# Kernel optimization log

Hardware: AMD Instinct MI355X
Metric: run time of the kernel (lower is better)

The kernel has to match this reference:

```python
import jax, jax.numpy as jnp
import numpy as np

N = 62      # EEG channels / graph nodes
F = 5       # features per node (frequency bands)
H = 64      # num_hiddens
C = 3       # num_classes
K = 2       # SGC propagation steps
B = 32768   # batch size
BN_EPS = 1e-5
NORM_EPS = 1e-10


def setup_inputs() -> dict:
    key = jax.random.key(0)
    ks = jax.random.split(key, 8)
    n_tril = N * (N + 1) // 2  # 1953 lower-tri (incl diag) learnable edge weights
    return {
        "X": jax.random.normal(ks[0], (B, N, F), dtype=jnp.float32),
        "edge_w_tril": jax.random.normal(ks[1], (n_tril,), dtype=jnp.float32),
        "bn_gamma": jnp.ones((F,), dtype=jnp.float32),
        "bn_beta": jnp.zeros((F,), dtype=jnp.float32),
        "lin_W": jax.random.normal(ks[2], (F, H), dtype=jnp.float32) * 0.1,
        "lin_b": jax.random.normal(ks[3], (H,), dtype=jnp.float32) * 0.1,
        "fc1_W": jax.random.normal(ks[4], (N * H, 64), dtype=jnp.float32) * 0.02,
        "fc1_b": jax.random.normal(ks[5], (64,), dtype=jnp.float32) * 0.02,
        "fc2_W": jax.random.normal(ks[6], (64, C), dtype=jnp.float32) * 0.1,
        "fc2_b": jax.random.normal(ks[7], (C,), dtype=jnp.float32) * 0.1,
    }


def _propagation_matrix(edge_w_tril):
    # Rebuild symmetric learnable adjacency from lower-tri params
    xs, ys = jnp.tril_indices(N)
    W = jnp.zeros((N, N), dtype=edge_w_tril.dtype).at[xs, ys].set(edge_w_tril)
    W = W + W.T - jnp.diag(jnp.diag(W))
    # normalize_A: relu + D^{-1/2} A D^{-1/2}
    A = jax.nn.relu(W)
    d = jnp.sum(A, axis=1)
    dinv = 1.0 / jnp.sqrt(d + NORM_EPS)
    L = dinv[:, None] * A * dinv[None, :]
    # NewSGConv.norm: add self-loops (weight 1), deg = row-sum of |w|,
    # norm_ij = deg_i^{-1/2} w_ij deg_j^{-1/2}. Dense form since edge list is all-pairs.
    deg = jnp.sum(jnp.abs(L), axis=1) + 1.0  # +1 from self-loop
    dis = 1.0 / jnp.sqrt(deg)                 # deg >= 1, no inf
    S = dis[:, None] * (L + jnp.eye(N, dtype=L.dtype)) * dis[None, :]
    return S


def _forward(X, edge_w_tril, bn_gamma, bn_beta, lin_W, lin_b, fc1_W, fc1_b, fc2_W, fc2_b):
    # BatchNorm1d over feature dim (training mode: batch stats over (B, N)), biased var
    mean = jnp.mean(X, axis=(0, 1))
    var = jnp.mean(jnp.square(X - mean), axis=(0, 1))
    x = (X - mean) / jnp.sqrt(var + BN_EPS) * bn_gamma + bn_beta  # (B, N, F)

    S = _propagation_matrix(edge_w_tril)  # (N, N)
    # K steps of SGC propagation: x <- S x (gather-scale-scatter == dense matmul here)
    for _ in range(K):
        x = jnp.einsum('ij,bjf->bif', S, x)
    x = jnp.einsum('bnf,fh->bnh', x, lin_W) + lin_b  # SGConv linear, (B, N, H)

    x = x.reshape(x.shape[0], -1)                    # (B, N*H)
    x = jax.nn.relu(x @ fc1_W + fc1_b)
    return x @ fc2_W + fc2_b                         # (B, C) logits


def reference(X, edge_w_tril, bn_gamma, bn_beta, lin_W, lin_b, fc1_W, fc1_b, fc2_W, fc2_b):
    return _forward(X, edge_w_tril, bn_gamma, bn_beta, lin_W, lin_b,
                    fc1_W, fc1_b, fc2_W, fc2_b)
```

## Files before the change

### kernel.cpp

```cpp
#include <hip/hip_runtime.h>
#include <math.h>


typedef __bf16 bf16_t;
typedef __attribute__((ext_vector_type(8))) __bf16 bf16x8;
typedef __attribute__((ext_vector_type(4))) float f32x4;

#define BN_COUNT 2031616.0f

__global__ __launch_bounds__(256) void k_conv(const float* __restrict__ X,
                                              const float* __restrict__ edge,
                                              float* __restrict__ part,
                                              bf16x8* __restrict__ Ahi,
                                              bf16x8* __restrict__ Alo,
                                              float* __restrict__ S2g)
{
    __shared__ float lds[32 * 312];
    const int t = threadIdx.x;
    if (blockIdx.x < 1024) {
        const float* Xb = X + (size_t)blockIdx.x * 32 * 310;
        float s0=0,s1=0,s2=0,s3=0,s4=0,q0=0,q1=0,q2=0,q3=0,q4=0;
        for (int i = t; i < 4960; i += 256) {
            int row = i / 155;
            int cc  = i - row * 155;
            float2 v = *reinterpret_cast<const float2*>(Xb + (size_t)row*310 + 2*cc);
            lds[row*312 + 2*cc]     = v.x;
            lds[row*312 + 2*cc + 1] = v.y;
            int f0 = (2*cc) % 5;
            int f1 = (f0 == 4) ? 0 : f0 + 1;
            float xx = v.x*v.x, yy = v.y*v.y;
            s0 += (f0==0)?v.x:0.f; s1 += (f0==1)?v.x:0.f; s2 += (f0==2)?v.x:0.f;
            s3 += (f0==3)?v.x:0.f; s4 += (f0==4)?v.x:0.f;
            q0 += (f0==0)?xx:0.f;  q1 += (f0==1)?xx:0.f;  q2 += (f0==2)?xx:0.f;
            q3 += (f0==3)?xx:0.f;  q4 += (f0==4)?xx:0.f;
            s0 += (f1==0)?v.y:0.f; s1 += (f1==1)?v.y:0.f; s2 += (f1==2)?v.y:0.f;
            s3 += (f1==3)?v.y:0.f; s4 += (f1==4)?v.y:0.f;
            q0 += (f1==0)?yy:0.f;  q1 += (f1==1)?yy:0.f;  q2 += (f1==2)?yy:0.f;
            q3 += (f1==3)?yy:0.f;  q4 += (f1==4)?yy:0.f;
        }
        float st[10] = {s0,s1,s2,s3,s4,q0,q1,q2,q3,q4};
#pragma unroll
        for (int k = 0; k < 10; ++k)
#pragma unroll
            for (int m = 32; m >= 1; m >>= 1) st[k] += __shfl_xor(st[k], m);
        __shared__ float red[4][10];
        int lane = t & 63, w = t >> 6;
        if (lane == 0)
#pragma unroll
            for (int k = 0; k < 10; ++k) red[w][k] = st[k];
        __syncthreads();
        if (t < 10)
            part[blockIdx.x*10 + t] = red[0][t] + red[1][t] + red[2][t] + red[3][t];
        const int mt0 = blockIdx.x * 2;
        for (int i = t; i < 1280; i += 256) {
            int mt   = i / 640;
            int rem  = i - mt * 640;
            int ks   = rem >> 6;
            int lane2 = rem & 63;
            int row  = (mt << 4) + (lane2 & 15);
            int k0   = ks * 32 + ((lane2 >> 4) << 3);
            bf16x8 h8, l8;
#pragma unroll
            for (int j = 0; j < 8; ++j) {
                int k = k0 + j;
                float val = (k < 310) ? lds[row*312 + k] : 0.f;
                __bf16 h = (__bf16)val;
                h8[j] = h;
                l8[j] = (__bf16)(val - (float)h);
            }
            size_t idx = (size_t)(mt0 + mt) * 640 + ks * 64 + lane2;
            Ahi[idx] = h8;
            Alo[idx] = l8;
        }
    } else {
        float* Sm  = lds;
        float* dv  = lds + 3968;
        float* dis = lds + 4032;
        for (int e = t; e < 3968; e += 256) {
            int i = e >> 6, j = e & 63;
            float v = 0.f;
            if (j < 62) {
                int idx = (i >= j) ? (i*(i+1)/2 + j) : (j*(j+1)/2 + i);
                v = fmaxf(edge[idx], 0.f);
            }
            Sm[e] = v;
        }
        __syncthreads();
        if (t < 62) {
            float s = 0.f;
            for (int j = 0; j < 64; ++j) s += Sm[t*64 + j];
            dv[t] = 1.0f / sqrtf(s + 1e-10f);
        }
        __syncthreads();
        for (int e = t; e < 3968; e += 256) {
            int i = e >> 6, j = e & 63;
            if (j < 62) Sm[e] *= dv[i] * dv[j];
        }
        __syncthreads();
        if (t < 62) {
            float dg = 1.0f;
            for (int j = 0; j < 64; ++j) dg += fabsf(Sm[t*64 + j]);
            dis[t] = 1.0f / sqrtf(dg);
        }
        __syncthreads();
        for (int e = t; e < 3968; e += 256) {
            int i = e >> 6, j = e & 63;
            if (j < 62) {
                float v = Sm[e] + ((i == j) ? 1.0f : 0.0f);
                Sm[e] = dis[i] * v * dis[j];
            }
        }
        __syncthreads();
        for (int g = t; g < 992; g += 256) {
            int i = g >> 4, j0 = (g & 15) << 2;
            float4 acc = {0.f, 0.f, 0.f, 0.f};
            for (int k = 0; k < 62; ++k) {
                float s = Sm[i*64 + k];
                float4 b = *reinterpret_cast<const float4*>(&Sm[k*64 + j0]);
                acc.x += s*b.x; acc.y += s*b.y; acc.z += s*b.z; acc.w += s*b.w;
            }
            *reinterpret_cast<float4*>(&S2g[i*64 + j0]) = acc;
        }
    }
}

__global__ __launch_bounds__(256) void k_setup(
    const float* __restrict__ part, const float* __restrict__ S2g,
    const float* __restrict__ gamma, const float* __restrict__ beta,
    const float* __restrict__ linW, const float* __restrict__ linb,
    const float* __restrict__ fc1W, const float* __restrict__ fc1b,
    float* __restrict__ MeffT, float* __restrict__ constv)
{
    const int o = blockIdx.x;
    const int t = threadIdx.x;
    __shared__ float S2m[3968];
    __shared__ float colo[3968];
    __shared__ float Tm[310];
    __shared__ float lw[320];
    __shared__ float scale[5], shift[5];
    __shared__ float redbuf[256];

    {
        float st[10];
#pragma unroll
        for (int k = 0; k < 10; ++k) st[k] = 0.f;
        for (int b = t; b < 1024; b += 256)
#pragma unroll
            for (int k = 0; k < 10; ++k) st[k] += part[b*10 + k];
#pragma unroll
        for (int k = 0; k < 10; ++k)
#pragma unroll
            for (int m = 32; m >= 1; m >>= 1) st[k] += __shfl_xor(st[k], m);
        int lane = t & 63, w = t >> 6;
        if (lane == 0)
            for (int k = 0; k < 10; ++k) redbuf[w*10 + k] = st[k];
    }
    for (int i = t; i < 3968; i += 256) {
        S2m[i]  = S2g[i];
        colo[i] = fc1W[(size_t)i*64 + o];
    }
    for (int i = t; i < 320; i += 256) lw[i] = linW[i];
    __syncthreads();

    if (t < 10)
        redbuf[64 + t] = redbuf[t] + redbuf[10+t] + redbuf[20+t] + redbuf[30+t];
    __syncthreads();
    if (t < 5) {
        float mean = redbuf[64 + t] * (1.0f / BN_COUNT);
        float var  = redbuf[69 + t] * (1.0f / BN_COUNT) - mean*mean;
        float inv  = 1.0f / sqrtf(var + 1e-5f);
        scale[t] = gamma[t] * inv;
        shift[t] = beta[t] - mean * gamma[t] * inv;
    }
    for (int p = t; p < 310; p += 256) {
        int n = p / 5, f = p - n*5;
        float sum = 0.f;
        for (int h = 0; h < 64; ++h) sum += lw[f*64 + h] * colo[n*64 + h];
        Tm[p] = sum;
    }
    __syncthreads();
    float cpart = 0.f;
    for (int p = t; p < 310; p += 256) {
        int j = p / 5, f = p - j*5;
        float m = 0.f;
        for (int n = 0; n < 62; ++n) m += S2m[n*64 + j] * Tm[n*5 + f];
        MeffT[o*320 + p] = scale[f] * m;
        cpart += shift[f] * m;
    }
    if (t < 10) MeffT[o*320 + 310 + t] = 0.f;
    for (int nh = t; nh < 3968; nh += 256)
        cpart += linb[nh & 63] * colo[nh];
    __syncthreads();
    redbuf[t] = cpart;
    __syncthreads();
    for (int sft = 128; sft > 0; sft >>= 1) {
        if (t < sft) redbuf[t] += redbuf[t + sft];
        __syncthreads();
    }
    if (t == 0) constv[o] = redbuf[0] + fc1b[o];
}

__global__ __launch_bounds__(64) void k_pack(const float* __restrict__ MeffT,
                                             bf16x8* __restrict__ Bhi,
                                             bf16x8* __restrict__ Blo)
{
    const int b  = blockIdx.x;
    const int nt = b / 10;
    const int ks = b - nt * 10;
    const int lane = threadIdx.x;
    const int col = nt*16 + (lane & 15);
    const int k0  = ks*32 + ((lane >> 4) << 3);
    bf16x8 h8, l8;
#pragma unroll
    for (int j = 0; j < 8; ++j) {
        float val = MeffT[col*320 + k0 + j];
        __bf16 h = (__bf16)val;
        h8[j] = h;
        l8[j] = (__bf16)(val - (float)h);
    }
    Bhi[(nt*10 + ks)*64 + lane] = h8;
    Blo[(nt*10 + ks)*64 + lane] = l8;
}

__global__ __launch_bounds__(256) void k_gemm(
    const bf16x8* __restrict__ Ahi, const bf16x8* __restrict__ Alo,
    const bf16x8* __restrict__ Bhi, const bf16x8* __restrict__ Blo,
    const float* __restrict__ constv, const float* __restrict__ fc2W,
    const float* __restrict__ fc2b, float* __restrict__ out)
{
    const int t = threadIdx.x;
    const int lane = t & 63;
    const int waveId = blockIdx.x * 4 + (t >> 6);
    const bf16x8* pAh = Ahi + (size_t)waveId * 1280 + lane;
    const bf16x8* pAl = Alo + (size_t)waveId * 1280 + lane;
    const bf16x8* pBh = Bhi + lane;
    const bf16x8* pBl = Blo + lane;

    f32x4 acc[2][4];
#pragma unroll
    for (int m = 0; m < 2; ++m)
#pragma unroll
        for (int n = 0; n < 4; ++n) acc[m][n] = (f32x4){0.f,0.f,0.f,0.f};

    bf16x8 ah[2][2], al[2][2], bh[2][4], bl[2][4];
#define LOAD_KS(B_, KS_) do {                                            \
        ah[B_][0] = pAh[(KS_)*64];        ah[B_][1] = pAh[640 + (KS_)*64]; \
        al[B_][0] = pAl[(KS_)*64];        al[B_][1] = pAl[640 + (KS_)*64]; \
        bh[B_][0] = pBh[(KS_)*64];        bh[B_][1] = pBh[(10+(KS_))*64];  \
        bh[B_][2] = pBh[(20+(KS_))*64];   bh[B_][3] = pBh[(30+(KS_))*64];  \
        bl[B_][0] = pBl[(KS_)*64];        bl[B_][1] = pBl[(10+(KS_))*64];  \
        bl[B_][2] = pBl[(20+(KS_))*64];   bl[B_][3] = pBl[(30+(KS_))*64];  \
    } while (0)

    LOAD_KS(0, 0);
#pragma unroll
    for (int ks = 0; ks < 10; ++ks) {
        if (ks < 9) {
            if ((ks & 1) == 0) LOAD_KS(1, ks + 1);
            else               LOAD_KS(0, ks + 1);
        }
        const int bb = ks & 1;
#pragma unroll
        for (int m = 0; m < 2; ++m)
#pragma unroll
            for (int n = 0; n < 4; ++n) {
                acc[m][n] = __builtin_amdgcn_mfma_f32_16x16x32_bf16(ah[bb][m], bh[bb][n], acc[m][n], 0, 0, 0);
                acc[m][n] = __builtin_amdgcn_mfma_f32_16x16x32_bf16(ah[bb][m], bl[bb][n], acc[m][n], 0, 0, 0);
                acc[m][n] = __builtin_amdgcn_mfma_f32_16x16x32_bf16(al[bb][m], bh[bb][n], acc[m][n], 0, 0, 0);
            }
    }
#undef LOAD_KS

    const int cl = lane & 15;
    float cst[4], f2r[4][3];
#pragma unroll
    for (int n = 0; n < 4; ++n) {
        int col = n*16 + cl;
        cst[n]    = constv[col];
        f2r[n][0] = fc2W[col*3 + 0];
        f2r[n][1] = fc2W[col*3 + 1];
        f2r[n][2] = fc2W[col*3 + 2];
    }
    float b0 = fc2b[0], b1 = fc2b[1], b2 = fc2b[2];
#pragma unroll
    for (int m = 0; m < 2; ++m) {
#pragma unroll
        for (int r = 0; r < 4; ++r) {
            float p0 = 0.f, p1 = 0.f, p2 = 0.f;
#pragma unroll
            for (int n = 0; n < 4; ++n) {
                float z = fmaxf(acc[m][n][r] + cst[n], 0.f);
                p0 += z * f2r[n][0];
                p1 += z * f2r[n][1];
                p2 += z * f2r[n][2];
            }
#pragma unroll
            for (int msk = 1; msk < 16; msk <<= 1) {
                p0 += __shfl_xor(p0, msk);
                p1 += __shfl_xor(p1, msk);
                p2 += __shfl_xor(p2, msk);
            }
            if (cl == 0) {
                int row = waveId*32 + m*16 + (lane >> 4)*4 + r;
                size_t rw = (size_t)row * 3;
                out[rw + 0] = p0 + b0;
                out[rw + 1] = p1 + b1;
                out[rw + 2] = p2 + b2;
            }
        }
    }
}

extern "C" void kernel_launch(void* const* d_in, const int* in_sizes, int n_in,
                              void* d_out, int out_size, void* d_ws, size_t ws_size,
                              hipStream_t stream)
{
    const float* X     = (const float*)d_in[0];
    const float* edge  = (const float*)d_in[1];
    const float* gamma = (const float*)d_in[2];
    const float* beta  = (const float*)d_in[3];
    const float* linW  = (const float*)d_in[4];
    const float* linb  = (const float*)d_in[5];
    const float* fc1W  = (const float*)d_in[6];
    const float* fc1b  = (const float*)d_in[7];
    const float* fc2W  = (const float*)d_in[8];
    const float* fc2b  = (const float*)d_in[9];
    float* out = (float*)d_out;
    float* ws  = (float*)d_ws;

    float*  part   = ws;
    float*  S2g    = ws + 10240;
    float*  MeffT  = ws + 14208;
    float*  constv = ws + 34688;
    bf16x8* Bhi    = (bf16x8*)(ws + 34816);
    bf16x8* Blo    = (bf16x8*)(ws + 45056);
    bf16x8* Ahi    = (bf16x8*)(ws + 65536);
    bf16x8* Alo    = (bf16x8*)(ws + 5308416);

    hipLaunchKernelGGL(k_conv,  dim3(1025), dim3(256), 0, stream,
                       X, edge, part, Ahi, Alo, S2g);
    hipLaunchKernelGGL(k_setup, dim3(64),   dim3(256), 0, stream,
                       part, S2g, gamma, beta, linW, linb, fc1W, fc1b, MeffT, constv);
    hipLaunchKernelGGL(k_pack,  dim3(40),   dim3(64),  0, stream, MeffT, Bhi, Blo);
    hipLaunchKernelGGL(k_gemm,  dim3(256),  dim3(256), 0, stream,
                       Ahi, Alo, Bhi, Blo, constv, fc2W, fc2b, out);
}
```

Measured before the change: 143.1 us.

## Read X directly in GEMM, drop A-staging buffers and fuse B packing into setup

The stats kernel now only computes BatchNorm partial sums with vectorized float4 loads, and no longer writes bf16 hi/lo copies of X to the workspace. The GEMM kernel loads X rows straight from global memory and splits them into hi/lo bf16 in registers. The separate pack kernel is gone because setup now writes the MFMA-layout B fragments directly. This removes a large intermediate write and reread plus one launch. In exchange X is read twice, the GEMM loads are uncoalesced float2 accesses with a 310-float row stride, and each wave now covers 16 rows instead of 32.

After: 129.2 us. 1.11x faster.

```diff
diff --git a/kernel.cpp b/kernel.cpp
--- a/kernel.cpp
+++ b/kernel.cpp
@@ -2,76 +2,46 @@
 #include <math.h>
 
 
-typedef __bf16 bf16_t;
 typedef __attribute__((ext_vector_type(8))) __bf16 bf16x8;
 typedef __attribute__((ext_vector_type(4))) float f32x4;
 
 #define BN_COUNT 2031616.0f
 
-__global__ __launch_bounds__(256) void k_conv(const float* __restrict__ X,
-                                              const float* __restrict__ edge,
-                                              float* __restrict__ part,
-                                              bf16x8* __restrict__ Ahi,
-                                              bf16x8* __restrict__ Alo,
-                                              float* __restrict__ S2g)
-{
-    __shared__ float lds[32 * 312];
+__global__ __launch_bounds__(256) void k_stats(const float* __restrict__ X,
+                                               const float* __restrict__ edge,
+                                               float* __restrict__ part,
+                                               float* __restrict__ S2g)
+{
+    __shared__ __align__(16) float lds[4160];
     const int t = threadIdx.x;
-    if (blockIdx.x < 1024) {
-        const float* Xb = X + (size_t)blockIdx.x * 32 * 310;
-        float s0=0,s1=0,s2=0,s3=0,s4=0,q0=0,q1=0,q2=0,q3=0,q4=0;
-        for (int i = t; i < 4960; i += 256) {
-            int row = i / 155;
-            int cc  = i - row * 155;
-            float2 v = *reinterpret_cast<const float2*>(Xb + (size_t)row*310 + 2*cc);
-            lds[row*312 + 2*cc]     = v.x;
-            lds[row*312 + 2*cc + 1] = v.y;
-            int f0 = (2*cc) % 5;
-            int f1 = (f0 == 4) ? 0 : f0 + 1;
-            float xx = v.x*v.x, yy = v.y*v.y;
-            s0 += (f0==0)?v.x:0.f; s1 += (f0==1)?v.x:0.f; s2 += (f0==2)?v.x:0.f;
-            s3 += (f0==3)?v.x:0.f; s4 += (f0==4)?v.x:0.f;
-            q0 += (f0==0)?xx:0.f;  q1 += (f0==1)?xx:0.f;  q2 += (f0==2)?xx:0.f;
-            q3 += (f0==3)?xx:0.f;  q4 += (f0==4)?xx:0.f;
-            s0 += (f1==0)?v.y:0.f; s1 += (f1==1)?v.y:0.f; s2 += (f1==2)?v.y:0.f;
-            s3 += (f1==3)?v.y:0.f; s4 += (f1==4)?v.y:0.f;
-            q0 += (f1==0)?yy:0.f;  q1 += (f1==1)?yy:0.f;  q2 += (f1==2)?yy:0.f;
-            q3 += (f1==3)?yy:0.f;  q4 += (f1==4)?yy:0.f;
-        }
-        float st[10] = {s0,s1,s2,s3,s4,q0,q1,q2,q3,q4};
-#pragma unroll
-        for (int k = 0; k < 10; ++k)
-#pragma unroll
-            for (int m = 32; m >= 1; m >>= 1) st[k] += __shfl_xor(st[k], m);
-        __shared__ float red[4][10];
+    if (blockIdx.x < 496) {
+        int tid = blockIdx.x * 256 + t;
+        const float4* Xv = reinterpret_cast<const float4*>(X) + (size_t)tid * 20;
+        float s[5] = {0.f,0.f,0.f,0.f,0.f};
+        float q[5] = {0.f,0.f,0.f,0.f,0.f};
+#pragma unroll
+        for (int v = 0; v < 20; ++v) {
+            float4 x = Xv[v];
+            s[(4*v+0)%5] += x.x; q[(4*v+0)%5] += x.x*x.x;
+            s[(4*v+1)%5] += x.y; q[(4*v+1)%5] += x.y*x.y;
+            s[(4*v+2)%5] += x.z; q[(4*v+2)%5] += x.z*x.z;
+            s[(4*v+3)%5] += x.w; q[(4*v+3)%5] += x.w*x.w;
+        }
+#pragma unroll
+        for (int k = 0; k < 5; ++k)
+#pragma unroll
+            for (int m = 32; m >= 1; m >>= 1) {
+                s[k] += __shfl_xor(s[k], m);
+                q[k] += __shfl_xor(q[k], m);
+            }
         int lane = t & 63, w = t >> 6;
-        if (lane == 0)
-#pragma unroll
-            for (int k = 0; k < 10; ++k) red[w][k] = st[k];
+        if (lane == 0) {
+#pragma unroll
+            for (int k = 0; k < 5; ++k) { lds[w*10+k] = s[k]; lds[w*10+5+k] = q[k]; }
+        }
         __syncthreads();
         if (t < 10)
-            part[blockIdx.x*10 + t] = red[0][t] + red[1][t] + red[2][t] + red[3][t];
-        const int mt0 = blockIdx.x * 2;
-        for (int i = t; i < 1280; i += 256) {
-            int mt   = i / 640;
-            int rem  = i - mt * 640;
-            int ks   = rem >> 6;
-            int lane2 = rem & 63;
-            int row  = (mt << 4) + (lane2 & 15);
-            int k0   = ks * 32 + ((lane2 >> 4) << 3);
-            bf16x8 h8, l8;
-#pragma unroll
-            for (int j = 0; j < 8; ++j) {
-                int k = k0 + j;
-                float val = (k < 310) ? lds[row*312 + k] : 0.f;
-                __bf16 h = (__bf16)val;
-                h8[j] = h;
-                l8[j] = (__bf16)(val - (float)h);
-            }
-            size_t idx = (size_t)(mt0 + mt) * 640 + ks * 64 + lane2;
-            Ahi[idx] = h8;
-            Alo[idx] = l8;
-        }
+            part[blockIdx.x*10 + t] = lds[t] + lds[10+t] + lds[20+t] + lds[30+t];
     } else {
         float* Sm  = lds;
         float* dv  = lds + 3968;
@@ -129,7 +99,8 @@
     const float* __restrict__ gamma, const float* __restrict__ beta,
     const float* __restrict__ linW, const float* __restrict__ linb,
     const float* __restrict__ fc1W, const float* __restrict__ fc1b,
-    float* __restrict__ MeffT, float* __restrict__ constv)
+    __bf16* __restrict__ Bhi, __bf16* __restrict__ Blo,
+    float* __restrict__ constv)
 {
     const int o = blockIdx.x;
     const int t = threadIdx.x;
@@ -144,7 +115,7 @@
         float st[10];
 #pragma unroll
         for (int k = 0; k < 10; ++k) st[k] = 0.f;
-        for (int b = t; b < 1024; b += 256)
+        for (int b = t; b < 496; b += 256)
 #pragma unroll
             for (int k = 0; k < 10; ++k) st[k] += part[b*10 + k];
 #pragma unroll
@@ -179,15 +150,30 @@
         Tm[p] = sum;
     }
     __syncthreads();
+    const int nt = o >> 4;
+    const int cl = o & 15;
     float cpart = 0.f;
     for (int p = t; p < 310; p += 256) {
-        int j = p / 5, f = p - j*5;
+        int nd = p / 5, f = p - nd*5;
         float m = 0.f;
-        for (int n = 0; n < 62; ++n) m += S2m[n*64 + j] * Tm[n*5 + f];
-        MeffT[o*320 + p] = scale[f] * m;
+        for (int n = 0; n < 62; ++n) m += S2m[n*64 + nd] * Tm[n*5 + f];
+        float val = scale[f] * m;
         cpart += shift[f] * m;
-    }
-    if (t < 10) MeffT[o*320 + 310 + t] = 0.f;
+        int ks = p >> 5, qq = (p >> 3) & 3, jj = p & 7;
+        int ln = (qq << 4) | cl;
+        size_t fo = ((size_t)(nt*10 + ks)*64 + ln)*8 + jj;
+        __bf16 h = (__bf16)val;
+        Bhi[fo] = h;
+        Blo[fo] = (__bf16)(val - (float)h);
+    }
+    if (t < 10) {
+        int p = 310 + t;
+        int ks = p >> 5, qq = (p >> 3) & 3, jj = p & 7;
+        int ln = (qq << 4) | cl;
+        size_t fo = ((size_t)(nt*10 + ks)*64 + ln)*8 + jj;
+        Bhi[fo] = (__bf16)0.f;
+        Blo[fo] = (__bf16)0.f;
+    }
     for (int nh = t; nh < 3968; nh += 256)
         cpart += linb[nh & 63] * colo[nh];
     __syncthreads();
@@ -200,30 +186,37 @@
     if (t == 0) constv[o] = redbuf[0] + fc1b[o];
 }
 
-__global__ __launch_bounds__(64) void k_pack(const float* __restrict__ MeffT,
-                                             bf16x8* __restrict__ Bhi,
-                                             bf16x8* __restrict__ Blo)
-{
-    const int b  = blockIdx.x;
-    const int nt = b / 10;
-    const int ks = b - nt * 10;
-    const int lane = threadIdx.x;
-    const int col = nt*16 + (lane & 15);
-    const int k0  = ks*32 + ((lane >> 4) << 3);
-    bf16x8 h8, l8;
+__device__ __forceinline__ void loadA(const float* __restrict__ xrow, int q,
+                                      int ks, bf16x8& ah, bf16x8& al)
+{
+    float v[8];
+    if (ks < 9 || q < 2) {
+        float2 a = *reinterpret_cast<const float2*>(xrow + ks*32);
+        float2 b = *reinterpret_cast<const float2*>(xrow + ks*32 + 2);
+        float2 c = *reinterpret_cast<const float2*>(xrow + ks*32 + 4);
+        float2 d = *reinterpret_cast<const float2*>(xrow + ks*32 + 6);
+        v[0]=a.x; v[1]=a.y; v[2]=b.x; v[3]=b.y;
+        v[4]=c.x; v[5]=c.y; v[6]=d.x; v[7]=d.y;
+    } else if (q == 2) {
+        float2 a = *reinterpret_cast<const float2*>(xrow + ks*32);
+        float2 b = *reinterpret_cast<const float2*>(xrow + ks*32 + 2);
+        float2 c = *reinterpret_cast<const float2*>(xrow + ks*32 + 4);
+        v[0]=a.x; v[1]=a.y; v[2]=b.x; v[3]=b.y;
+        v[4]=c.x; v[5]=c.y; v[6]=0.f; v[7]=0.f;
+    } else {
+#pragma unroll
+        for (int j = 0; j < 8; ++j) v[j] = 0.f;
+    }
 #pragma unroll
     for (int j = 0; j < 8; ++j) {
-        float val = MeffT[col*320 + k0 + j];
-        __bf16 h = (__bf16)val;
-        h8[j] = h;
-        l8[j] = (__bf16)(val - (float)h);
-    }
-    Bhi[(nt*10 + ks)*64 + lane] = h8;
-    Blo[(nt*10 + ks)*64 + lane] = l8;
+        __bf16 h = (__bf16)v[j];
+        ah[j] = h;
+        al[j] = (__bf16)(v[j] - (float)h);
+    }
 }
 
 __global__ __launch_bounds__(256) void k_gemm(
-    const bf16x8* __restrict__ Ahi, const bf16x8* __restrict__ Alo,
+    const float* __restrict__ X,
     const bf16x8* __restrict__ Bhi, const bf16x8* __restrict__ Blo,
     const float* __restrict__ constv, const float* __restrict__ fc2W,
     const float* __restrict__ fc2b, float* __restrict__ out)
@@ -231,51 +224,46 @@
     const int t = threadIdx.x;
     const int lane = t & 63;
     const int waveId = blockIdx.x * 4 + (t >> 6);
-    const bf16x8* pAh = Ahi + (size_t)waveId * 1280 + lane;
-    const bf16x8* pAl = Alo + (size_t)waveId * 1280 + lane;
+    const int rl = lane & 15;
+    const int q  = lane >> 4;
+    const float* xrow = X + (size_t)(waveId*16 + rl)*310 + q*8;
     const bf16x8* pBh = Bhi + lane;
     const bf16x8* pBl = Blo + lane;
 
-    f32x4 acc[2][4];
-#pragma unroll
-    for (int m = 0; m < 2; ++m)
-#pragma unroll
-        for (int n = 0; n < 4; ++n) acc[m][n] = (f32x4){0.f,0.f,0.f,0.f};
-
-    bf16x8 ah[2][2], al[2][2], bh[2][4], bl[2][4];
-#define LOAD_KS(B_, KS_) do {                                            \
-        ah[B_][0] = pAh[(KS_)*64];        ah[B_][1] = pAh[640 + (KS_)*64]; \
-        al[B_][0] = pAl[(KS_)*64];        al[B_][1] = pAl[640 + (KS_)*64]; \
-        bh[B_][0] = pBh[(KS_)*64];        bh[B_][1] = pBh[(10+(KS_))*64];  \
-        bh[B_][2] = pBh[(20+(KS_))*64];   bh[B_][3] = pBh[(30+(KS_))*64];  \
-        bl[B_][0] = pBl[(KS_)*64];        bl[B_][1] = pBl[(10+(KS_))*64];  \
-        bl[B_][2] = pBl[(20+(KS_))*64];   bl[B_][3] = pBl[(30+(KS_))*64];  \
+    f32x4 acc[4];
+#pragma unroll
+    for (int n = 0; n < 4; ++n) acc[n] = (f32x4){0.f,0.f,0.f,0.f};
+
+    bf16x8 ah[2], al[2], bh[2][4], bl[2][4];
+#define LOAD_B(B_, KS_) do {                                              \
+        bh[B_][0] = pBh[(KS_)*64];        bh[B_][1] = pBh[(10+(KS_))*64]; \
+        bh[B_][2] = pBh[(20+(KS_))*64];   bh[B_][3] = pBh[(30+(KS_))*64]; \
+        bl[B_][0] = pBl[(KS_)*64];        bl[B_][1] = pBl[(10+(KS_))*64]; \
+        bl[B_][2] = pBl[(20+(KS_))*64];   bl[B_][3] = pBl[(30+(KS_))*64]; \
     } while (0)
 
-    LOAD_KS(0, 0);
+    loadA(xrow, q, 0, ah[0], al[0]);
+    LOAD_B(0, 0);
 #pragma unroll
     for (int ks = 0; ks < 10; ++ks) {
+        const int cur = ks & 1, nxt = cur ^ 1;
         if (ks < 9) {
-            if ((ks & 1) == 0) LOAD_KS(1, ks + 1);
-            else               LOAD_KS(0, ks + 1);
-        }
-        const int bb = ks & 1;
-#pragma unroll
-        for (int m = 0; m < 2; ++m)
-#pragma unroll
-            for (int n = 0; n < 4; ++n) {
-                acc[m][n] = __builtin_amdgcn_mfma_f32_16x16x32_bf16(ah[bb][m], bh[bb][n], acc[m][n], 0, 0, 0);
-                acc[m][n] = __builtin_amdgcn_mfma_f32_16x16x32_bf16(ah[bb][m], bl[bb][n], acc[m][n], 0, 0, 0);
-                acc[m][n] = __builtin_amdgcn_mfma_f32_16x16x32_bf16(al[bb][m], bh[bb][n], acc[m][n], 0, 0, 0);
-            }
-    }
-#undef LOAD_KS
-
-    const int cl = lane & 15;
+            loadA(xrow, q, ks + 1, ah[nxt], al[nxt]);
+            LOAD_B(nxt, ks + 1);
+        }
+#pragma unroll
+        for (int n = 0; n < 4; ++n) {
+            acc[n] = __builtin_amdgcn_mfma_f32_16x16x32_bf16(ah[cur], bh[cur][n], acc[n], 0, 0, 0);
+            acc[n] = __builtin_amdgcn_mfma_f32_16x16x32_bf16(ah[cur], bl[cur][n], acc[n], 0, 0, 0);
+            acc[n] = __builtin_amdgcn_mfma_f32_16x16x32_bf16(al[cur], bh[cur][n], acc[n], 0, 0, 0);
+        }
+    }
+#undef LOAD_B
+
     float cst[4], f2r[4][3];
 #pragma unroll
     for (int n = 0; n < 4; ++n) {
-        int col = n*16 + cl;
+        int col = n*16 + rl;
         cst[n]    = constv[col];
         f2r[n][0] = fc2W[col*3 + 0];
         f2r[n][1] = fc2W[col*3 + 1];
@@ -283,30 +271,27 @@
     }
     float b0 = fc2b[0], b1 = fc2b[1], b2 = fc2b[2];
 #pragma unroll
-    for (int m = 0; m < 2; ++m) {
-#pragma unroll
-        for (int r = 0; r < 4; ++r) {
-            float p0 = 0.f, p1 = 0.f, p2 = 0.f;
-#pragma unroll
-            for (int n = 0; n < 4; ++n) {
-                float z = fmaxf(acc[m][n][r] + cst[n], 0.f);
-                p0 += z * f2r[n][0];
-                p1 += z * f2r[n][1];
-                p2 += z * f2r[n][2];
-            }
-#pragma unroll
-            for (int msk = 1; msk < 16; msk <<= 1) {
-                p0 += __shfl_xor(p0, msk);
-                p1 += __shfl_xor(p1, msk);
-                p2 += __shfl_xor(p2, msk);
-            }
-            if (cl == 0) {
-                int row = waveId*32 + m*16 + (lane >> 4)*4 + r;
-                size_t rw = (size_t)row * 3;
-                out[rw + 0] = p0 + b0;
-                out[rw + 1] = p1 + b1;
-                out[rw + 2] = p2 + b2;
-            }
+    for (int r = 0; r < 4; ++r) {
+        float p0 = 0.f, p1 = 0.f, p2 = 0.f;
+#pragma unroll
+        for (int n = 0; n < 4; ++n) {
+            float z = fmaxf(acc[n][r] + cst[n], 0.f);
+            p0 += z * f2r[n][0];
+            p1 += z * f2r[n][1];
+            p2 += z * f2r[n][2];
+        }
+#pragma unroll
+        for (int msk = 1; msk < 16; msk <<= 1) {
+            p0 += __shfl_xor(p0, msk);
+            p1 += __shfl_xor(p1, msk);
+            p2 += __shfl_xor(p2, msk);
+        }
+        if (rl == 0) {
+            int row = waveId*16 + q*4 + r;
+            size_t rw = (size_t)row * 3;
+            out[rw + 0] = p0 + b0;
+            out[rw + 1] = p1 + b1;
+            out[rw + 2] = p2 + b2;
         }
     }
 }
@@ -329,19 +314,15 @@
     float* ws  = (float*)d_ws;
 
     float*  part   = ws;
-    float*  S2g    = ws + 10240;
-    float*  MeffT  = ws + 14208;
-    float*  constv = ws + 34688;
-    bf16x8* Bhi    = (bf16x8*)(ws + 34816);
-    bf16x8* Blo    = (bf16x8*)(ws + 45056);
-    bf16x8* Ahi    = (bf16x8*)(ws + 65536);
-    bf16x8* Alo    = (bf16x8*)(ws + 5308416);
-
-    hipLaunchKernelGGL(k_conv,  dim3(1025), dim3(256), 0, stream,
-                       X, edge, part, Ahi, Alo, S2g);
-    hipLaunchKernelGGL(k_setup, dim3(64),   dim3(256), 0, stream,
-                       part, S2g, gamma, beta, linW, linb, fc1W, fc1b, MeffT, constv);
-    hipLaunchKernelGGL(k_pack,  dim3(40),   dim3(64),  0, stream, MeffT, Bhi, Blo);
-    hipLaunchKernelGGL(k_gemm,  dim3(256),  dim3(256), 0, stream,
-                       Ahi, Alo, Bhi, Blo, constv, fc2W, fc2b, out);
-}
+    float*  S2g    = ws + 4960;
+    float*  constv = ws + 8928;
+    __bf16* Bhi    = (__bf16*)(ws + 8992);
+    __bf16* Blo    = (__bf16*)(ws + 19232);
+
+    hipLaunchKernelGGL(k_stats, dim3(497), dim3(256), 0, stream, X, edge, part, S2g);
+    hipLaunchKernelGGL(k_setup, dim3(64),  dim3(256), 0, stream,
+                       part, S2g, gamma, beta, linW, linb, fc1W, fc1b, Bhi, Blo, constv);
+    hipLaunchKernelGGL(k_gemm,  dim3(512), dim3(256), 0, stream,
+                       X, (const bf16x8*)Bhi, (const bf16x8*)Blo,
+                       constv, fc2W, fc2b, out);
+}
```
